# Optimization experiments

Hardware: AMD Instinct MI355X
Metric: run time of the kernel (lower is better)

## Reference

```python
import jax, jax.numpy as jnp
import numpy as np

NUM_GRAPHS = 128
NODES_PER_GRAPH = 512
NUM_NODES = NUM_GRAPHS * NODES_PER_GRAPH
NUM_EDGES = NUM_NODES * 16
IN_DIM = 64
HID = 128
NUM_HEADS = 4
BN_EPS = 1e-5


def setup_inputs() -> dict:
    key = jax.random.key(0)
    ks = jax.random.split(key, 12)
    x = jax.random.normal(ks[0], (NUM_NODES, IN_DIM), dtype=jnp.float32)
    edge_index = jax.random.randint(ks[1], (2, NUM_EDGES), 0, NUM_NODES, dtype=jnp.int32)
    batch = jnp.repeat(jnp.arange(NUM_GRAPHS, dtype=jnp.int32), NODES_PER_GRAPH)
    s = 0.05
    W0 = jax.random.normal(ks[2], (IN_DIM, HID), dtype=jnp.float32) * s
    b0 = jnp.zeros((HID,), jnp.float32)
    Wh = jax.random.normal(ks[3], (3, HID, HID), dtype=jnp.float32) * s  # convs 1..3
    bh = jnp.zeros((3, HID), jnp.float32)
    bn_gamma = jnp.ones((4, HID), jnp.float32)
    bn_beta = jnp.zeros((4, HID), jnp.float32)
    bn_mean = jnp.zeros((4, HID), jnp.float32)
    bn_var = jnp.ones((4, HID), jnp.float32)
    attn_in_w = jax.random.normal(ks[4], (3 * HID, HID), dtype=jnp.float32) * s
    attn_in_b = jnp.zeros((3 * HID,), jnp.float32)
    attn_out_w = jax.random.normal(ks[5], (HID, HID), dtype=jnp.float32) * s
    attn_out_b = jnp.zeros((HID,), jnp.float32)
    return dict(x=x, W0=W0, b0=b0, Wh=Wh, bh=bh, bn_gamma=bn_gamma, bn_beta=bn_beta,
                bn_mean=bn_mean, bn_var=bn_var, attn_in_w=attn_in_w, attn_in_b=attn_in_b,
                attn_out_w=attn_out_w, attn_out_b=attn_out_b, edge_index=edge_index, batch=batch)


def _forward(x, W0, b0, Wh, bh, bn_gamma, bn_beta, bn_mean, bn_var,
             attn_in_w, attn_in_b, attn_out_w, attn_out_b, edge_index, batch):
    N = x.shape[0]
    src, dst = edge_index[0], edge_index[1]
    # GCN symmetric normalization with self-loops (PyG GCNConv)
    deg = jax.ops.segment_sum(jnp.ones_like(src, jnp.float32), dst, num_segments=N) + 1.0
    dis = jax.lax.rsqrt(deg)                      # deg^{-1/2}
    enorm = (dis[src] * dis[dst])[:, None]        # per-edge norm
    self_norm = (dis * dis)[:, None]              # self-loop norm

    def gcn(h, W, b):
        h = h @ W
        agg = jax.ops.segment_sum(h[src] * enorm, dst, num_segments=N)
        return agg + h * self_norm + b

    def bn(h, i):
        scale = bn_gamma[i] * jax.lax.rsqrt(bn_var[i] + BN_EPS)
        return (h - bn_mean[i]) * scale + bn_beta[i]  # eval-mode BN

    # dropout is identity in eval mode
    h = jax.nn.relu(bn(gcn(x, W0, b0), 0))
    h = jax.nn.relu(bn(gcn(h, Wh[0], bh[0]), 1))
    h = jax.nn.relu(bn(gcn(h, Wh[1], bh[1]), 2))
    f = jax.nn.relu(bn(gcn(h, Wh[2], bh[2]), 3))   # [N, HID]

    # per-graph self-attention (equal-size contiguous graphs -> batched MHA)
    dh = HID // NUM_HEADS
    xg = f.reshape(NUM_GRAPHS, NODES_PER_GRAPH, HID)
    qkv = xg @ attn_in_w.T + attn_in_b            # [G, n, 3H]
    q, k, v = jnp.split(qkv, 3, axis=-1)

    def heads(t):
        return t.reshape(NUM_GRAPHS, NODES_PER_GRAPH, NUM_HEADS, dh).transpose(0, 2, 1, 3)
    q, k, v = heads(q), heads(k), heads(v)
    scores = jnp.einsum('ghnd,ghmd->ghnm', q, k) / np.sqrt(dh).astype(np.float32)
    attn = jax.nn.softmax(scores, axis=-1)
    o = jnp.einsum('ghnm,ghmd->ghnd', attn, v).transpose(0, 2, 1, 3).reshape(NUM_GRAPHS, NODES_PER_GRAPH, HID)
    o = o @ attn_out_w.T + attn_out_b
    final = o.reshape(N, HID)

    # global mean pool over batch indices
    cnt = jax.ops.segment_sum(jnp.ones((N,), jnp.float32), batch, num_segments=NUM_GRAPHS)
    graph_emb = jax.ops.segment_sum(final, batch, num_segments=NUM_GRAPHS) / cnt[:, None]
    return final, graph_emb


def reference(x, W0, b0, Wh, bh, bn_gamma, bn_beta, bn_mean, bn_var,
              attn_in_w, attn_in_b, attn_out_w, attn_out_b, edge_index, batch):
    return _forward(x, W0, b0, Wh, bh, bn_gamma, bn_beta, bn_mean, bn_var,
                    attn_in_w, attn_in_b, attn_out_w, attn_out_b, edge_index, batch)
```

## Files before the change

### kernel.cpp

```cpp
#include <hip/hip_runtime.h>
#include <hip/hip_bf16.h>
#include <cstdint>
#include <cstddef>

#define N_NODES 65536
#define N_EDGES 1048576
#define N_GRAPHS 128
#define NPG 512
#define IN_DIM 64
#define HID 128
#define BN_EPS 1e-5f

typedef __attribute__((ext_vector_type(8))) short bf16x8;
typedef __attribute__((ext_vector_type(4))) float f32x4;
typedef __attribute__((ext_vector_type(8))) unsigned short u16x8;

__device__ inline unsigned short f2bf(float f) {
  unsigned u = __builtin_bit_cast(unsigned, f);
  u = u + 0x7fffu + ((u >> 16) & 1u);
  return (unsigned short)(u >> 16);
}
__device__ inline float bf2f(unsigned short h) {
  unsigned u = ((unsigned)h) << 16;
  return __builtin_bit_cast(float, u);
}
__device__ inline void split_bf(float v, unsigned short& hi, unsigned short& lo) {
  hi = f2bf(v);
  lo = f2bf(v - bf2f(hi));
}

__global__ __launch_bounds__(256) void hist_kernel(const int* __restrict__ dst,
                                                   int* __restrict__ deg) {
  int e = blockIdx.x * 256 + threadIdx.x;
  if (e < N_EDGES) atomicAdd(&deg[dst[e]], 1);
}

__global__ __launch_bounds__(256) void dis_kernel(const int* __restrict__ deg,
                                                  float* __restrict__ dis) {
  int n = blockIdx.x * 256 + threadIdx.x;
  if (n < N_NODES) dis[n] = 1.0f / sqrtf((float)deg[n] + 1.0f);
}

__global__ __launch_bounds__(1024) void scan_kernel(const int* __restrict__ deg,
                                                    int* __restrict__ offsets,
                                                    int* __restrict__ cursor) {
  __shared__ int sums[1024];
  int t = threadIdx.x;
  int base = t * 64;
  const int4* dp = (const int4*)(deg + base);
  int s = 0;
#pragma unroll
  for (int i = 0; i < 16; i++) {
    int4 v = dp[i];
    s += v.x + v.y + v.z + v.w;
  }
  sums[t] = s;
  __syncthreads();
  for (int off = 1; off < 1024; off <<= 1) {
    int v = (t >= off) ? sums[t - off] : 0;
    __syncthreads();
    sums[t] += v;
    __syncthreads();
  }
  int run = (t == 0) ? 0 : sums[t - 1];
#pragma unroll
  for (int i = 0; i < 16; i++) {
    int4 v = dp[i];
    int idx = base + i * 4;
    offsets[idx] = run; cursor[idx] = run; run += v.x;
    offsets[idx + 1] = run; cursor[idx + 1] = run; run += v.y;
    offsets[idx + 2] = run; cursor[idx + 2] = run; run += v.z;
    offsets[idx + 3] = run; cursor[idx + 3] = run; run += v.w;
  }
  if (t == 1023) offsets[N_NODES] = run;
}

__global__ __launch_bounds__(256) void fill_kernel(const int* __restrict__ src,
                                                   const int* __restrict__ dst,
                                                   int* __restrict__ cursor,
                                                   int* __restrict__ csr) {
  int e = blockIdx.x * 256 + threadIdx.x;
  if (e < N_EDGES) {
    int d = dst[e];
    int slot = atomicAdd(&cursor[d], 1);
    csr[slot] = src[e];
  }
}

__global__ __launch_bounds__(256) void agg64_kernel(const float* __restrict__ x,
                                                    const float* __restrict__ dis,
                                                    const int* __restrict__ offsets,
                                                    const int* __restrict__ csr,
                                                    unsigned short* __restrict__ zhi,
                                                    unsigned short* __restrict__ zlo) {
  int node = blockIdx.x * 4 + (threadIdx.x >> 6);
  int lane = threadIdx.x & 63;
  float dn = dis[node];
  float acc = x[(size_t)node * 64 + lane] * dn * dn;
  int beg = offsets[node], end = offsets[node + 1];
  int k = beg;
  for (; k + 4 <= end; k += 4) {
    int s0 = csr[k], s1 = csr[k + 1], s2 = csr[k + 2], s3 = csr[k + 3];
    float w0 = dn * dis[s0], w1 = dn * dis[s1], w2 = dn * dis[s2], w3 = dn * dis[s3];
    float v0 = x[(size_t)s0 * 64 + lane];
    float v1 = x[(size_t)s1 * 64 + lane];
    float v2 = x[(size_t)s2 * 64 + lane];
    float v3 = x[(size_t)s3 * 64 + lane];
    acc = fmaf(w0, v0, acc);
    acc = fmaf(w1, v1, acc);
    acc = fmaf(w2, v2, acc);
    acc = fmaf(w3, v3, acc);
  }
  for (; k < end; k++) {
    int s = csr[k];
    acc = fmaf(dn * dis[s], x[(size_t)s * 64 + lane], acc);
  }
  unsigned short h_, l_;
  split_bf(acc, h_, l_);
  zhi[(size_t)node * 64 + lane] = h_;
  zlo[(size_t)node * 64 + lane] = l_;
}

__global__ __launch_bounds__(256) void agg128_kernel(const float* __restrict__ h,
                                                     const float* __restrict__ dis,
                                                     const int* __restrict__ offsets,
                                                     const int* __restrict__ csr,
                                                     unsigned short* __restrict__ zhi,
                                                     unsigned short* __restrict__ zlo) {
  int node = blockIdx.x * 4 + (threadIdx.x >> 6);
  int lane = threadIdx.x & 63;
  float dn = dis[node];
  float sn = dn * dn;
  const float* hr = h + (size_t)node * 128;
  float a0 = hr[lane] * sn;
  float a1 = hr[lane + 64] * sn;
  int beg = offsets[node], end = offsets[node + 1];
  int k = beg;
  for (; k + 4 <= end; k += 4) {
    int s0 = csr[k], s1 = csr[k + 1], s2 = csr[k + 2], s3 = csr[k + 3];
    float w0 = dn * dis[s0], w1 = dn * dis[s1], w2 = dn * dis[s2], w3 = dn * dis[s3];
    const float* p0 = h + (size_t)s0 * 128;
    const float* p1 = h + (size_t)s1 * 128;
    const float* p2 = h + (size_t)s2 * 128;
    const float* p3 = h + (size_t)s3 * 128;
    float u0 = p0[lane], d0 = p0[lane + 64];
    float u1 = p1[lane], d1 = p1[lane + 64];
    float u2 = p2[lane], d2 = p2[lane + 64];
    float u3 = p3[lane], d3 = p3[lane + 64];
    a0 = fmaf(w0, u0, a0); a1 = fmaf(w0, d0, a1);
    a0 = fmaf(w1, u1, a0); a1 = fmaf(w1, d1, a1);
    a0 = fmaf(w2, u2, a0); a1 = fmaf(w2, d2, a1);
    a0 = fmaf(w3, u3, a0); a1 = fmaf(w3, d3, a1);
  }
  for (; k < end; k++) {
    int s = csr[k];
    float w = dn * dis[s];
    const float* hs = h + (size_t)s * 128;
    a0 = fmaf(w, hs[lane], a0);
    a1 = fmaf(w, hs[lane + 64], a1);
  }
  unsigned short h0, l0, h1, l1;
  split_bf(a0, h0, l0);
  split_bf(a1, h1, l1);
  zhi[(size_t)node * 128 + lane] = h0;
  zlo[(size_t)node * 128 + lane] = l0;
  zhi[(size_t)node * 128 + lane + 64] = h1;
  zlo[(size_t)node * 128 + lane + 64] = l1;
}

template <bool TRANS>
__global__ __launch_bounds__(256) void wprep_kernel(const float* __restrict__ W, int K, int O,
                                                    unsigned short* __restrict__ hi,
                                                    unsigned short* __restrict__ lo) {
  int idx = blockIdx.x * 256 + threadIdx.x;
  int KC = K / 32;
  int total = (O / 16) * KC * 64;
  if (idx >= total) return;
  int lane = idx & 63;
  int rest = idx >> 6;
  int kc = rest % KC;
  int nt = rest / KC;
  int n = nt * 16 + (lane & 15);
  int kb = kc * 32 + (lane >> 4) * 8;
  unsigned short* hp = hi + (size_t)idx * 8;
  unsigned short* lp = lo + (size_t)idx * 8;
#pragma unroll
  for (int j = 0; j < 8; j++) {
    int k = kb + j;
    float v = TRANS ? W[(size_t)n * K + k] : W[(size_t)k * O + n];
    unsigned short h_, l_;
    split_bf(v, h_, l_);
    hp[j] = h_;
    lp[j] = l_;
  }
}

template <int K, int O, bool DOBN, bool DORELU, bool SPLIT_OUT>
__global__ __launch_bounds__(256) void gemm_mfma(
    const unsigned short* __restrict__ Ahi, const unsigned short* __restrict__ Alo,
    const unsigned short* __restrict__ Whi, const unsigned short* __restrict__ Wlo,
    const float* __restrict__ bias,
    const float* __restrict__ gamma, const float* __restrict__ beta,
    const float* __restrict__ mean, const float* __restrict__ var,
    float* __restrict__ Cf, unsigned short* __restrict__ Chi,
    unsigned short* __restrict__ Clo) {
  constexpr int KC = K / 32;
  int wave = threadIdx.x >> 6;
  int lane = threadIdx.x & 63;
  int m0 = blockIdx.x * 128 + wave * 32;
  int o0 = blockIdx.y * 128;
  int mrow = lane & 15;
  int kseg = (lane >> 4) * 8;

  f32x4 acc[2][8];
#pragma unroll
  for (int mt = 0; mt < 2; mt++)
#pragma unroll
    for (int nt = 0; nt < 8; nt++) acc[mt][nt] = (f32x4)0.0f;

#pragma unroll
  for (int kc = 0; kc < KC; kc++) {
    bf16x8 ah[2], al[2];
#pragma unroll
    for (int mt = 0; mt < 2; mt++) {
      size_t aoff = (size_t)(m0 + mt * 16 + mrow) * K + kc * 32 + kseg;
      ah[mt] = *(const bf16x8*)(Ahi + aoff);
      al[mt] = *(const bf16x8*)(Alo + aoff);
    }
#pragma unroll
    for (int nt = 0; nt < 8; nt++) {
      size_t foff = (((size_t)(blockIdx.y * 8 + nt) * KC + kc) * 64 + lane) * 8;
      bf16x8 bh = *(const bf16x8*)(Whi + foff);
      bf16x8 bl = *(const bf16x8*)(Wlo + foff);
#pragma unroll
      for (int mt = 0; mt < 2; mt++) {
        acc[mt][nt] = __builtin_amdgcn_mfma_f32_16x16x32_bf16(ah[mt], bh, acc[mt][nt], 0, 0, 0);
        acc[mt][nt] = __builtin_amdgcn_mfma_f32_16x16x32_bf16(ah[mt], bl, acc[mt][nt], 0, 0, 0);
        acc[mt][nt] = __builtin_amdgcn_mfma_f32_16x16x32_bf16(al[mt], bh, acc[mt][nt], 0, 0, 0);
        acc[mt][nt] = __builtin_amdgcn_mfma_f32_16x16x32_bf16(al[mt], bl, acc[mt][nt], 0, 0, 0);
      }
    }
  }

  int ccol = lane & 15;
  int crow0 = (lane >> 4) * 4;
#pragma unroll
  for (int nt = 0; nt < 8; nt++) {
    int c = o0 + nt * 16 + ccol;
    float sc, cb;
    float b = bias[c];
    if (DOBN) {
      sc = gamma[c] * rsqrtf(var[c] + BN_EPS);
      cb = (b - mean[c]) * sc + beta[c];
    } else {
      sc = 1.0f;
      cb = b;
    }
#pragma unroll
    for (int mt = 0; mt < 2; mt++) {
#pragma unroll
      for (int r = 0; r < 4; r++) {
        float v = fmaf(acc[mt][nt][r], sc, cb);
        if (DORELU) v = fmaxf(v, 0.0f);
        size_t row = (size_t)(m0 + mt * 16 + crow0 + r);
        if (SPLIT_OUT) {
          unsigned short h_, l_;
          split_bf(v, h_, l_);
          Chi[row * O + c] = h_;
          Clo[row * O + c] = l_;
        } else {
          Cf[row * O + c] = v;
        }
      }
    }
  }
}

__global__ __launch_bounds__(256) void knorm_kernel(const float* __restrict__ qkv,
                                                    float* __restrict__ kmax2) {
  int g = blockIdx.x >> 2;
  int h = blockIdx.x & 3;
  size_t gbase = (size_t)g * NPG;
  float best = 0.0f;
#pragma unroll
  for (int r = 0; r < 2; r++) {
    int j = r * 256 + threadIdx.x;
    const float* kp = &qkv[(gbase + j) * 384 + 128 + h * 32];
    float s = 0.0f;
#pragma unroll
    for (int i = 0; i < 8; i++) {
      float4 v = *(const float4*)(kp + i * 4);
      s = fmaf(v.x, v.x, s);
      s = fmaf(v.y, v.y, s);
      s = fmaf(v.z, v.z, s);
      s = fmaf(v.w, v.w, s);
    }
    best = fmaxf(best, s);
  }
#pragma unroll
  for (int off = 32; off >= 1; off >>= 1)
    best = fmaxf(best, __shfl_xor(best, off, 64));
  __shared__ float red[4];
  int wave = threadIdx.x >> 6;
  if ((threadIdx.x & 63) == 0) red[wave] = best;
  __syncthreads();
  if (threadIdx.x == 0) {
    float m = fmaxf(fmaxf(red[0], red[1]), fmaxf(red[2], red[3]));
    kmax2[blockIdx.x] = m;
  }
}

__global__ __launch_bounds__(256, 2) void attn_kernel(const float* __restrict__ qkv,
                                                      const float* __restrict__ kmax2,
                                                      unsigned short* __restrict__ ohi,
                                                      unsigned short* __restrict__ olo) {
  int g = blockIdx.x >> 2;
  int h = blockIdx.x & 3;
  int t = threadIdx.x;
  int wave = t >> 6;
  int lane = t & 63;
  int pr = lane & 31;
  int hi16 = lane >> 5;
  size_t gbase = (size_t)g * NPG;

  const float cf = 0.17677669529663687f * 1.4426950408889634f;

  __shared__ float sk[128][36];
  __shared__ float sv[128][36];

  float q[4][16], o[4][16];
  float M[4], l[4];
  float km2 = kmax2[g * 4 + h];
#pragma unroll
  for (int m = 0; m < 4; m++) {
    int qi = wave * 128 + m * 32 + pr;
    const float* qp = &qkv[(gbase + qi) * 384 + h * 32 + hi16 * 16];
    float n = 0.0f;
#pragma unroll
    for (int i = 0; i < 4; i++) {
      float4 v = *(const float4*)(qp + i * 4);
      q[m][i * 4 + 0] = v.x * cf;
      q[m][i * 4 + 1] = v.y * cf;
      q[m][i * 4 + 2] = v.z * cf;
      q[m][i * 4 + 3] = v.w * cf;
    }
#pragma unroll
    for (int d = 0; d < 16; d++) n = fmaf(q[m][d], q[m][d], n);
    n += __shfl_xor(n, 32);
    M[m] = sqrtf(n * km2);
    l[m] = 0.0f;
#pragma unroll
    for (int d = 0; d < 16; d++) o[m][d] = 0.0f;
  }

  int srow = t & 127;
  int iskv = t >> 7;

  for (int c = 0; c < 4; c++) {
    __syncthreads();
    {
      const float* gp = &qkv[(gbase + (size_t)(c * 128 + srow)) * 384 + 128 +
                             iskv * 128 + h * 32];
      float* sp = iskv ? &sv[srow][0] : &sk[srow][0];
#pragma unroll
      for (int i = 0; i < 8; i++) *(float4*)(sp + i * 4) = *(const float4*)(gp + i * 4);
    }
    __syncthreads();
#pragma unroll 2
    for (int j = 0; j < 128; j++) {
      const float* kp = &sk[j][hi16 * 16];
      float4 k0 = *(const float4*)(kp);
      float4 k1 = *(const float4*)(kp + 4);
      float4 k2 = *(const float4*)(kp + 8);
      float4 k3 = *(const float4*)(kp + 12);
      float p[4];
#pragma unroll
      for (int m = 0; m < 4; m++) {
        float s0 = fmaf(q[m][3], k0.w, fmaf(q[m][2], k0.z, fmaf(q[m][1], k0.y, q[m][0] * k0.x)));
        float s1 = fmaf(q[m][7], k1.w, fmaf(q[m][6], k1.z, fmaf(q[m][5], k1.y, q[m][4] * k1.x)));
        float s2 = fmaf(q[m][11], k2.w, fmaf(q[m][10], k2.z, fmaf(q[m][9], k2.y, q[m][8] * k2.x)));
        float s3 = fmaf(q[m][15], k3.w, fmaf(q[m][14], k3.z, fmaf(q[m][13], k3.y, q[m][12] * k3.x)));
        float s = (s0 + s1) + (s2 + s3);
        s += __shfl_xor(s, 32);
        p[m] = __builtin_exp2f(s - M[m]);
        l[m] += p[m];
      }
      const float* vp = &sv[j][hi16 * 16];
      float4 v0 = *(const float4*)(vp);
      float4 v1 = *(const float4*)(vp + 4);
      float4 v2 = *(const float4*)(vp + 8);
      float4 v3 = *(const float4*)(vp + 12);
#pragma unroll
      for (int m = 0; m < 4; m++) {
        float pm = p[m];
        o[m][0] = fmaf(pm, v0.x, o[m][0]);   o[m][1] = fmaf(pm, v0.y, o[m][1]);
        o[m][2] = fmaf(pm, v0.z, o[m][2]);   o[m][3] = fmaf(pm, v0.w, o[m][3]);
        o[m][4] = fmaf(pm, v1.x, o[m][4]);   o[m][5] = fmaf(pm, v1.y, o[m][5]);
        o[m][6] = fmaf(pm, v1.z, o[m][6]);   o[m][7] = fmaf(pm, v1.w, o[m][7]);
        o[m][8] = fmaf(pm, v2.x, o[m][8]);   o[m][9] = fmaf(pm, v2.y, o[m][9]);
        o[m][10] = fmaf(pm, v2.z, o[m][10]); o[m][11] = fmaf(pm, v2.w, o[m][11]);
        o[m][12] = fmaf(pm, v3.x, o[m][12]); o[m][13] = fmaf(pm, v3.y, o[m][13]);
        o[m][14] = fmaf(pm, v3.z, o[m][14]); o[m][15] = fmaf(pm, v3.w, o[m][15]);
      }
    }
  }

#pragma unroll
  for (int m = 0; m < 4; m++) {
    float inv = 1.0f / l[m];
    int qi = wave * 128 + m * 32 + pr;
    size_t base = (gbase + qi) * 128 + h * 32 + hi16 * 16;
    u16x8 vh, vl;
#pragma unroll
    for (int half = 0; half < 2; half++) {
#pragma unroll
      for (int j2 = 0; j2 < 8; j2++) {
        unsigned short h_, l_;
        split_bf(o[m][half * 8 + j2] * inv, h_, l_);
        vh[j2] = h_;
        vl[j2] = l_;
      }
      *(u16x8*)(ohi + base + half * 8) = vh;
      *(u16x8*)(olo + base + half * 8) = vl;
    }
  }
}

__global__ __launch_bounds__(128) void pool_kernel(const float* __restrict__ fin,
                                                   float* __restrict__ emb) {
  int g = blockIdx.x, c = threadIdx.x;
  const float* p = fin + (size_t)g * NPG * HID + c;
  float s = 0.0f;
  for (int i = 0; i < NPG; i++) s += p[(size_t)i * HID];
  emb[g * HID + c] = s * (1.0f / NPG);
}

extern "C" void kernel_launch(void* const* d_in, const int* in_sizes, int n_in,
                              void* d_out, int out_size, void* d_ws, size_t ws_size,
                              hipStream_t stream) {
  (void)in_sizes; (void)n_in; (void)out_size; (void)ws_size;
  const float* x          = (const float*)d_in[0];
  const float* W0         = (const float*)d_in[1];
  const float* b0         = (const float*)d_in[2];
  const float* Wh         = (const float*)d_in[3];
  const float* bh         = (const float*)d_in[4];
  const float* bn_gamma   = (const float*)d_in[5];
  const float* bn_beta    = (const float*)d_in[6];
  const float* bn_mean    = (const float*)d_in[7];
  const float* bn_var     = (const float*)d_in[8];
  const float* attn_in_w  = (const float*)d_in[9];
  const float* attn_in_b  = (const float*)d_in[10];
  const float* attn_out_w = (const float*)d_in[11];
  const float* attn_out_b = (const float*)d_in[12];
  const int* edge_index   = (const int*)d_in[13];
  const int* src = edge_index;
  const int* dst = edge_index + N_EDGES;

  char* ws = (char*)d_ws;
  size_t off = 0;
  auto alloc = [&](size_t bytes) -> void* {
    void* p = ws + off;
    off += (bytes + 255) & ~(size_t)255;
    return p;
  };
  int*   deg     = (int*)alloc((size_t)N_NODES * 4);
  int*   offsets = (int*)alloc((size_t)(N_NODES + 1) * 4);
  int*   cursor  = (int*)alloc((size_t)N_NODES * 4);
  int*   csr     = (int*)alloc((size_t)N_EDGES * 4);
  float* dis     = (float*)alloc((size_t)N_NODES * 4);
  float* bufA    = (float*)alloc((size_t)N_NODES * HID * 4);
  unsigned short* zhi = (unsigned short*)alloc((size_t)N_NODES * HID * 2);
  unsigned short* zlo = (unsigned short*)alloc((size_t)N_NODES * HID * 2);
  float* qkvb    = (float*)alloc((size_t)N_NODES * 384 * 4);
  float* kmax2   = (float*)alloc((size_t)N_GRAPHS * 4 * 4);
  unsigned short* w0h = (unsigned short*)alloc(8192 * 2);
  unsigned short* w0l = (unsigned short*)alloc(8192 * 2);
  unsigned short* whh[3], *whl[3];
  for (int i = 0; i < 3; i++) {
    whh[i] = (unsigned short*)alloc(16384 * 2);
    whl[i] = (unsigned short*)alloc(16384 * 2);
  }
  unsigned short* wqh = (unsigned short*)alloc(49152 * 2);
  unsigned short* wql = (unsigned short*)alloc(49152 * 2);
  unsigned short* woh = (unsigned short*)alloc(16384 * 2);
  unsigned short* wol = (unsigned short*)alloc(16384 * 2);

  unsigned short* fhi = (unsigned short*)bufA;
  unsigned short* flo = fhi + (size_t)N_NODES * HID;

  float* fin = (float*)d_out;
  float* emb = fin + (size_t)N_NODES * HID;

  hipMemsetAsync(deg, 0, (size_t)N_NODES * 4, stream);
  hist_kernel<<<N_EDGES / 256, 256, 0, stream>>>(dst, deg);
  dis_kernel<<<N_NODES / 256, 256, 0, stream>>>(deg, dis);
  scan_kernel<<<1, 1024, 0, stream>>>(deg, offsets, cursor);
  fill_kernel<<<N_EDGES / 256, 256, 0, stream>>>(src, dst, cursor, csr);

  wprep_kernel<false><<<4, 256, 0, stream>>>(W0, 64, 128, w0h, w0l);
  for (int i = 0; i < 3; i++)
    wprep_kernel<false><<<8, 256, 0, stream>>>(Wh + (size_t)i * HID * HID, 128, 128,
                                               whh[i], whl[i]);
  wprep_kernel<true><<<24, 256, 0, stream>>>(attn_in_w, 128, 384, wqh, wql);
  wprep_kernel<true><<<8, 256, 0, stream>>>(attn_out_w, 128, 128, woh, wol);

  dim3 ggrid(N_NODES / 128, 1);
  agg64_kernel<<<N_NODES / 4, 256, 0, stream>>>(x, dis, offsets, csr, zhi, zlo);
  gemm_mfma<64, 128, true, true, false><<<ggrid, 256, 0, stream>>>(
      zhi, zlo, w0h, w0l, b0, bn_gamma, bn_beta, bn_mean, bn_var, bufA, nullptr, nullptr);
  for (int L = 0; L < 2; L++) {
    agg128_kernel<<<N_NODES / 4, 256, 0, stream>>>(bufA, dis, offsets, csr, zhi, zlo);
    gemm_mfma<128, 128, true, true, false><<<ggrid, 256, 0, stream>>>(
        zhi, zlo, whh[L], whl[L], bh + (size_t)L * HID,
        bn_gamma + (size_t)(L + 1) * HID, bn_beta + (size_t)(L + 1) * HID,
        bn_mean + (size_t)(L + 1) * HID, bn_var + (size_t)(L + 1) * HID,
        bufA, nullptr, nullptr);
  }
  agg128_kernel<<<N_NODES / 4, 256, 0, stream>>>(bufA, dis, offsets, csr, zhi, zlo);
  gemm_mfma<128, 128, true, true, true><<<ggrid, 256, 0, stream>>>(
      zhi, zlo, whh[2], whl[2], bh + (size_t)2 * HID,
      bn_gamma + (size_t)3 * HID, bn_beta + (size_t)3 * HID,
      bn_mean + (size_t)3 * HID, bn_var + (size_t)3 * HID,
      nullptr, fhi, flo);
  dim3 qgrid(N_NODES / 128, 3);
  gemm_mfma<128, 384, false, false, false><<<qgrid, 256, 0, stream>>>(
      fhi, flo, wqh, wql, attn_in_b, nullptr, nullptr, nullptr, nullptr,
      qkvb, nullptr, nullptr);
  knorm_kernel<<<N_GRAPHS * 4, 256, 0, stream>>>(qkvb, kmax2);
  attn_kernel<<<N_GRAPHS * 4, 256, 0, stream>>>(qkvb, kmax2, zhi, zlo);
  gemm_mfma<128, 128, false, false, false><<<ggrid, 256, 0, stream>>>(
      zhi, zlo, woh, wol, attn_out_b, nullptr, nullptr, nullptr, nullptr,
      fin, nullptr, nullptr);
  pool_kernel<<<N_GRAPHS, 128, 0, stream>>>(fin, emb);
}
```

Measured before the change: 997.2 us.

## Rewrite graph attention kernel to use bf16x3 MFMA for QK and PV

New measurement: 838.2 us. 15.9% less time.

```diff
diff --git a/kernel.cpp b/kernel.cpp
--- a/kernel.cpp
+++ b/kernel.cpp
@@ -310,118 +310,198 @@
   }
 }
 
-__global__ __launch_bounds__(256, 2) void attn_kernel(const float* __restrict__ qkv,
-                                                      const float* __restrict__ kmax2,
-                                                      unsigned short* __restrict__ ohi,
-                                                      unsigned short* __restrict__ olo) {
-  int g = blockIdx.x >> 2;
-  int h = blockIdx.x & 3;
+__global__ __launch_bounds__(256, 2) void attn_mfma_kernel(
+    const float* __restrict__ qkv, const float* __restrict__ kmax2,
+    unsigned short* __restrict__ ohi, unsigned short* __restrict__ olo) {
+  int b = blockIdx.x;
+  int g = b >> 3;
+  int h = (b >> 1) & 3;
+  int half = b & 1;
   int t = threadIdx.x;
   int wave = t >> 6;
   int lane = t & 63;
-  int pr = lane & 31;
-  int hi16 = lane >> 5;
+  int quad = lane >> 4;
+  int l15 = lane & 15;
   size_t gbase = (size_t)g * NPG;
+  int qb = half * 256 + wave * 64;
 
   const float cf = 0.17677669529663687f * 1.4426950408889634f;
 
-  __shared__ float sk[128][36];
-  __shared__ float sv[128][36];
-
-  float q[4][16], o[4][16];
-  float M[4], l[4];
+  __shared__ unsigned short Kh[32][40], Kl[32][40];
+  __shared__ unsigned short Vh[33][40], Vl[33][40];
+  __shared__ char wbuf[4][10240] __attribute__((aligned(16)));
+
+  unsigned short* Ph = (unsigned short*)wbuf[wave];
+  unsigned short* Pl = Ph + 64 * 40;
+  float* Ot = (float*)wbuf[wave];
+
+  bf16x8 qh[4], ql[4];
+  float qn2p[4];
+#pragma unroll
+  for (int mt = 0; mt < 4; mt++) {
+    const float* qp = &qkv[(gbase + qb + mt * 16 + l15) * 384 + h * 32 + quad * 8];
+    float4 f0 = *(const float4*)qp;
+    float4 f1 = *(const float4*)(qp + 4);
+    float v[8] = {f0.x * cf, f0.y * cf, f0.z * cf, f0.w * cf,
+                  f1.x * cf, f1.y * cf, f1.z * cf, f1.w * cf};
+    u16x8 hh, ll;
+    float s = 0.0f;
+#pragma unroll
+    for (int j = 0; j < 8; j++) {
+      unsigned short hi_, lo_;
+      split_bf(v[j], hi_, lo_);
+      hh[j] = hi_;
+      ll[j] = lo_;
+      s = fmaf(v[j], v[j], s);
+    }
+    qh[mt] = __builtin_bit_cast(bf16x8, hh);
+    ql[mt] = __builtin_bit_cast(bf16x8, ll);
+    s += __shfl_xor(s, 16);
+    s += __shfl_xor(s, 32);
+    qn2p[mt] = s;
+  }
+  if (quad == 0) {
+#pragma unroll
+    for (int mt = 0; mt < 4; mt++) Ot[mt * 16 + l15] = qn2p[mt];
+  }
   float km2 = kmax2[g * 4 + h];
-#pragma unroll
-  for (int m = 0; m < 4; m++) {
-    int qi = wave * 128 + m * 32 + pr;
-    const float* qp = &qkv[(gbase + qi) * 384 + h * 32 + hi16 * 16];
-    float n = 0.0f;
-#pragma unroll
-    for (int i = 0; i < 4; i++) {
-      float4 v = *(const float4*)(qp + i * 4);
-      q[m][i * 4 + 0] = v.x * cf;
-      q[m][i * 4 + 1] = v.y * cf;
-      q[m][i * 4 + 2] = v.z * cf;
-      q[m][i * 4 + 3] = v.w * cf;
-    }
-#pragma unroll
-    for (int d = 0; d < 16; d++) n = fmaf(q[m][d], q[m][d], n);
-    n += __shfl_xor(n, 32);
-    M[m] = sqrtf(n * km2);
-    l[m] = 0.0f;
-#pragma unroll
-    for (int d = 0; d < 16; d++) o[m][d] = 0.0f;
-  }
-
-  int srow = t & 127;
-  int iskv = t >> 7;
-
-  for (int c = 0; c < 4; c++) {
+  float Mq[4][4];
+#pragma unroll
+  for (int mt = 0; mt < 4; mt++)
+#pragma unroll
+    for (int r = 0; r < 4; r++)
+      Mq[mt][r] = sqrtf(Ot[mt * 16 + quad * 4 + r] * km2);
+
+  f32x4 Oa[4][3];
+#pragma unroll
+  for (int mt = 0; mt < 4; mt++)
+#pragma unroll
+    for (int nt = 0; nt < 3; nt++) Oa[mt][nt] = (f32x4)0.0f;
+
+  for (int c = 0; c < 16; c++) {
     __syncthreads();
-    {
-      const float* gp = &qkv[(gbase + (size_t)(c * 128 + srow)) * 384 + 128 +
-                             iskv * 128 + h * 32];
-      float* sp = iskv ? &sv[srow][0] : &sk[srow][0];
-#pragma unroll
-      for (int i = 0; i < 8; i++) *(float4*)(sp + i * 4) = *(const float4*)(gp + i * 4);
+    if (t >= 128) {
+      int t2 = t - 128;
+      int key = t2 >> 2;
+      int ds = (t2 & 3) * 8;
+      const float* kp = &qkv[(gbase + (size_t)(c * 32 + key)) * 384 + 128 + h * 32 + ds];
+      float4 f0 = *(const float4*)kp;
+      float4 f1 = *(const float4*)(kp + 4);
+      float v[8] = {f0.x, f0.y, f0.z, f0.w, f1.x, f1.y, f1.z, f1.w};
+      u16x8 hh, ll;
+#pragma unroll
+      for (int j = 0; j < 8; j++) {
+        unsigned short hi_, lo_;
+        split_bf(v[j], hi_, lo_);
+        hh[j] = hi_;
+        ll[j] = lo_;
+      }
+      *(u16x8*)&Kh[key][ds] = hh;
+      *(u16x8*)&Kl[key][ds] = ll;
+    } else if (t < 64) {
+      int keyb = (t & 7) * 4;
+      int dvb = (t >> 3) * 4;
+      float4 r0 = *(const float4*)&qkv[(gbase + (size_t)(c * 32 + keyb + 0)) * 384 + 256 + h * 32 + dvb];
+      float4 r1 = *(const float4*)&qkv[(gbase + (size_t)(c * 32 + keyb + 1)) * 384 + 256 + h * 32 + dvb];
+      float4 r2 = *(const float4*)&qkv[(gbase + (size_t)(c * 32 + keyb + 2)) * 384 + 256 + h * 32 + dvb];
+      float4 r3 = *(const float4*)&qkv[(gbase + (size_t)(c * 32 + keyb + 3)) * 384 + 256 + h * 32 + dvb];
+      float rr[4][4] = {{r0.x, r0.y, r0.z, r0.w}, {r1.x, r1.y, r1.z, r1.w},
+                        {r2.x, r2.y, r2.z, r2.w}, {r3.x, r3.y, r3.z, r3.w}};
+#pragma unroll
+      for (int c2 = 0; c2 < 4; c2++) {
+        ushort4 hv, lv;
+        unsigned short hi_, lo_;
+        split_bf(rr[0][c2], hi_, lo_); hv.x = hi_; lv.x = lo_;
+        split_bf(rr[1][c2], hi_, lo_); hv.y = hi_; lv.y = lo_;
+        split_bf(rr[2][c2], hi_, lo_); hv.z = hi_; lv.z = lo_;
+        split_bf(rr[3][c2], hi_, lo_); hv.w = hi_; lv.w = lo_;
+        *(ushort4*)&Vh[dvb + c2][keyb] = hv;
+        *(ushort4*)&Vl[dvb + c2][keyb] = lv;
+      }
+    } else if (t < 68) {
+      int i = t - 64;
+      u16x8 ones;
+#pragma unroll
+      for (int j = 0; j < 8; j++) ones[j] = 0x3F80;
+      *(u16x8*)&Vh[32][i * 8] = ones;
     }
     __syncthreads();
-#pragma unroll 2
-    for (int j = 0; j < 128; j++) {
-      const float* kp = &sk[j][hi16 * 16];
-      float4 k0 = *(const float4*)(kp);
-      float4 k1 = *(const float4*)(kp + 4);
-      float4 k2 = *(const float4*)(kp + 8);
-      float4 k3 = *(const float4*)(kp + 12);
-      float p[4];
-#pragma unroll
-      for (int m = 0; m < 4; m++) {
-        float s0 = fmaf(q[m][3], k0.w, fmaf(q[m][2], k0.z, fmaf(q[m][1], k0.y, q[m][0] * k0.x)));
-        float s1 = fmaf(q[m][7], k1.w, fmaf(q[m][6], k1.z, fmaf(q[m][5], k1.y, q[m][4] * k1.x)));
-        float s2 = fmaf(q[m][11], k2.w, fmaf(q[m][10], k2.z, fmaf(q[m][9], k2.y, q[m][8] * k2.x)));
-        float s3 = fmaf(q[m][15], k3.w, fmaf(q[m][14], k3.z, fmaf(q[m][13], k3.y, q[m][12] * k3.x)));
-        float s = (s0 + s1) + (s2 + s3);
-        s += __shfl_xor(s, 32);
-        p[m] = __builtin_exp2f(s - M[m]);
-        l[m] += p[m];
+
+#pragma unroll
+    for (int nt = 0; nt < 2; nt++) {
+      bf16x8 bkh = *(const bf16x8*)&Kh[nt * 16 + l15][quad * 8];
+      bf16x8 bkl = *(const bf16x8*)&Kl[nt * 16 + l15][quad * 8];
+#pragma unroll
+      for (int mt = 0; mt < 4; mt++) {
+        f32x4 S = (f32x4)0.0f;
+        S = __builtin_amdgcn_mfma_f32_16x16x32_bf16(qh[mt], bkh, S, 0, 0, 0);
+        S = __builtin_amdgcn_mfma_f32_16x16x32_bf16(qh[mt], bkl, S, 0, 0, 0);
+        S = __builtin_amdgcn_mfma_f32_16x16x32_bf16(ql[mt], bkh, S, 0, 0, 0);
+        S = __builtin_amdgcn_mfma_f32_16x16x32_bf16(ql[mt], bkl, S, 0, 0, 0);
+#pragma unroll
+        for (int r = 0; r < 4; r++) {
+          float p = __builtin_exp2f(S[r] - Mq[mt][r]);
+          unsigned short hi_, lo_;
+          split_bf(p, hi_, lo_);
+          int row = mt * 16 + quad * 4 + r;
+          Ph[row * 40 + nt * 16 + l15] = hi_;
+          Pl[row * 40 + nt * 16 + l15] = lo_;
+        }
       }
-      const float* vp = &sv[j][hi16 * 16];
-      float4 v0 = *(const float4*)(vp);
-      float4 v1 = *(const float4*)(vp + 4);
-      float4 v2 = *(const float4*)(vp + 8);
-      float4 v3 = *(const float4*)(vp + 12);
-#pragma unroll
-      for (int m = 0; m < 4; m++) {
-        float pm = p[m];
-        o[m][0] = fmaf(pm, v0.x, o[m][0]);   o[m][1] = fmaf(pm, v0.y, o[m][1]);
-        o[m][2] = fmaf(pm, v0.z, o[m][2]);   o[m][3] = fmaf(pm, v0.w, o[m][3]);
-        o[m][4] = fmaf(pm, v1.x, o[m][4]);   o[m][5] = fmaf(pm, v1.y, o[m][5]);
-        o[m][6] = fmaf(pm, v1.z, o[m][6]);   o[m][7] = fmaf(pm, v1.w, o[m][7]);
-        o[m][8] = fmaf(pm, v2.x, o[m][8]);   o[m][9] = fmaf(pm, v2.y, o[m][9]);
-        o[m][10] = fmaf(pm, v2.z, o[m][10]); o[m][11] = fmaf(pm, v2.w, o[m][11]);
-        o[m][12] = fmaf(pm, v3.x, o[m][12]); o[m][13] = fmaf(pm, v3.y, o[m][13]);
-        o[m][14] = fmaf(pm, v3.z, o[m][14]); o[m][15] = fmaf(pm, v3.w, o[m][15]);
+    }
+    bf16x8 pah[4], pal[4];
+#pragma unroll
+    for (int mt = 0; mt < 4; mt++) {
+      pah[mt] = *(const bf16x8*)&Ph[(mt * 16 + l15) * 40 + quad * 8];
+      pal[mt] = *(const bf16x8*)&Pl[(mt * 16 + l15) * 40 + quad * 8];
+    }
+#pragma unroll
+    for (int nt = 0; nt < 3; nt++) {
+      bf16x8 bvh = *(const bf16x8*)&Vh[nt * 16 + l15][quad * 8];
+      if (nt < 2) {
+        bf16x8 bvl = *(const bf16x8*)&Vl[nt * 16 + l15][quad * 8];
+#pragma unroll
+        for (int mt = 0; mt < 4; mt++) {
+          Oa[mt][nt] = __builtin_amdgcn_mfma_f32_16x16x32_bf16(pah[mt], bvh, Oa[mt][nt], 0, 0, 0);
+          Oa[mt][nt] = __builtin_amdgcn_mfma_f32_16x16x32_bf16(pah[mt], bvl, Oa[mt][nt], 0, 0, 0);
+          Oa[mt][nt] = __builtin_amdgcn_mfma_f32_16x16x32_bf16(pal[mt], bvh, Oa[mt][nt], 0, 0, 0);
+        }
+      } else {
+#pragma unroll
+        for (int mt = 0; mt < 4; mt++) {
+          Oa[mt][nt] = __builtin_amdgcn_mfma_f32_16x16x32_bf16(pah[mt], bvh, Oa[mt][nt], 0, 0, 0);
+          Oa[mt][nt] = __builtin_amdgcn_mfma_f32_16x16x32_bf16(pal[mt], bvh, Oa[mt][nt], 0, 0, 0);
+        }
       }
     }
   }
 
 #pragma unroll
-  for (int m = 0; m < 4; m++) {
-    float inv = 1.0f / l[m];
-    int qi = wave * 128 + m * 32 + pr;
-    size_t base = (gbase + qi) * 128 + h * 32 + hi16 * 16;
+  for (int mt = 0; mt < 4; mt++) {
+#pragma unroll
+    for (int r = 0; r < 4; r++) {
+      int row = mt * 16 + quad * 4 + r;
+      Ot[row * 36 + l15] = Oa[mt][0][r];
+      Ot[row * 36 + 16 + l15] = Oa[mt][1][r];
+      if (l15 == 0) Ot[row * 36 + 32] = Oa[mt][2][r];
+    }
+  }
+  {
+    int row = lane;
+    float inv = 1.0f / Ot[row * 36 + 32];
+    size_t node = gbase + qb + row;
     u16x8 vh, vl;
 #pragma unroll
-    for (int half = 0; half < 2; half++) {
-#pragma unroll
-      for (int j2 = 0; j2 < 8; j2++) {
-        unsigned short h_, l_;
-        split_bf(o[m][half * 8 + j2] * inv, h_, l_);
-        vh[j2] = h_;
-        vl[j2] = l_;
+    for (int seg = 0; seg < 4; seg++) {
+#pragma unroll
+      for (int j = 0; j < 8; j++) {
+        unsigned short hi_, lo_;
+        split_bf(Ot[row * 36 + seg * 8 + j] * inv, hi_, lo_);
+        vh[j] = hi_;
+        vl[j] = lo_;
       }
-      *(u16x8*)(ohi + base + half * 8) = vh;
-      *(u16x8*)(olo + base + half * 8) = vl;
+      *(u16x8*)(ohi + node * 128 + h * 32 + seg * 8) = vh;
+      *(u16x8*)(olo + node * 128 + h * 32 + seg * 8) = vl;
     }
   }
 }
@@ -527,7 +607,7 @@
       fhi, flo, wqh, wql, attn_in_b, nullptr, nullptr, nullptr, nullptr,
       qkvb, nullptr, nullptr);
   knorm_kernel<<<N_GRAPHS * 4, 256, 0, stream>>>(qkvb, kmax2);
-  attn_kernel<<<N_GRAPHS * 4, 256, 0, stream>>>(qkvb, kmax2, zhi, zlo);
+  attn_mfma_kernel<<<N_GRAPHS * 4 * 2, 256, 0, stream>>>(qkvb, kmax2, zhi, zlo);
   gemm_mfma<128, 128, false, false, false><<<ggrid, 256, 0, stream>>>(
       zhi, zlo, woh, wol, attn_out_b, nullptr, nullptr, nullptr, nullptr,
       fin, nullptr, nullptr);
```
